# Kernel tuning notes

Measured on AMD Instinct MI355X. Metric: run time of the kernel, lower is better.

## Reference

```python
import jax, jax.numpy as jnp
import numpy as np

N = 100000
E = 1600000
D = 128


def setup_inputs() -> dict:
    key = jax.random.key(0)
    ks = jax.random.split(key, 9)
    s = 1.0 / np.sqrt(D)
    return {
        "x": jax.random.normal(ks[0], (N, D), dtype=jnp.float32),
        "edge_index": jax.random.randint(ks[1], (2, E), 0, N, dtype=jnp.int64),
        # SAGEConv layer 1: lin_l (neighbor path, with bias), lin_r (root path, no bias)
        "Wl1": jax.random.normal(ks[2], (D, D), dtype=jnp.float32) * s,
        "bl1": jnp.zeros((D,), dtype=jnp.float32),
        "Wr1": jax.random.normal(ks[3], (D, D), dtype=jnp.float32) * s,
        # SAGEConv layer 2
        "Wl2": jax.random.normal(ks[4], (D, D), dtype=jnp.float32) * s,
        "bl2": jnp.zeros((D,), dtype=jnp.float32),
        "Wr2": jax.random.normal(ks[5], (D, D), dtype=jnp.float32) * s,
    }


def _sage_conv(x, src, dst, Wl, bl, Wr):
    # PyG SAGEConv, aggr='mean', root_weight=True:
    #   out = lin_l(mean_{j in N(i)} x_j) + lin_r(x_i)
    msg = x[src]                                              # [E, D] gather
    agg = jax.ops.segment_sum(msg, dst, num_segments=N)       # [N, D]
    cnt = jax.ops.segment_sum(jnp.ones((src.shape[0],), x.dtype), dst, num_segments=N)
    agg = agg / jnp.maximum(cnt, 1.0)[:, None]                # mean aggregation
    return agg @ Wl.T + bl + x @ Wr.T


def reference(x, edge_index, Wl1, bl1, Wr1, Wl2, bl2, Wr2):
    src, dst = edge_index[0], edge_index[1]
    h = jax.nn.relu(_sage_conv(x, src, dst, Wl1, bl1, Wr1))
    out = _sage_conv(h, src, dst, Wl2, bl2, Wr2)
    return out
```

## Files before the change

### kernel.cpp

```cpp
#include <hip/hip_runtime.h>
#include <stdint.h>

#define DN 128
#define NBITS 6
#define BNODES 64
#define HBMAX 2048
#define CAP 1536
#define NSL 256

__host__ __device__ static inline int divup(int a, int b){ return (a+b-1)/b; }

typedef __attribute__((ext_vector_type(8))) short bf16x8;
typedef __attribute__((ext_vector_type(4))) float floatx4;

__device__ __forceinline__ unsigned short f2bf(float f){
  unsigned int x = __float_as_uint(f);
  unsigned int r = x + 0x7fffu + ((x >> 16) & 1u);
  return (unsigned short)(r >> 16);
}
__device__ __forceinline__ unsigned int pack2(unsigned short a, unsigned short b){
  return (unsigned int)a | ((unsigned int)b << 16);
}

__global__ __launch_bounds__(256)
void convert_scatter(const float* __restrict__ x,
                     const float* __restrict__ w0, const float* __restrict__ w1,
                     const float* __restrict__ w2, const float* __restrict__ w3,
                     unsigned short* __restrict__ xb, unsigned short* __restrict__ Wb,
                     const int* __restrict__ src, const int* __restrict__ dst,
                     int* __restrict__ gcur, unsigned int* __restrict__ packed,
                     int E, int nbuck, int count8){
  __shared__ int h[HBMAX];
  __shared__ int cur[HBMAX];
  int t = threadIdx.x;

  if (blockIdx.x < NSL){
    int s = blockIdx.x;
    for (int i=t; i<nbuck; i+=256) h[i] = 0;
    __syncthreads();
    int n4 = E >> 2, per4 = divup(n4, NSL);
    int lo = s*per4, hi = min(lo+per4, n4);
    const int4* dst4 = (const int4*)dst;
    for (int i = lo + t; i < hi; i += 256){
      int4 d4 = dst4[i];
      atomicAdd(&h[d4.x >> NBITS], 1);
      atomicAdd(&h[d4.y >> NBITS], 1);
      atomicAdd(&h[d4.z >> NBITS], 1);
      atomicAdd(&h[d4.w >> NBITS], 1);
    }
    if (s == NSL-1){
      for (int e = (n4<<2) + t; e < E; e += 256)
        atomicAdd(&h[dst[e] >> NBITS], 1);
    }
    __syncthreads();
    for (int i=t; i<nbuck; i+=256){
      int c = h[i];
      int base = c ? atomicAdd(&gcur[i], c) : 0;
      cur[i] = i*CAP + base;
    }
    __syncthreads();
    const int4* src4 = (const int4*)src;
    for (int i = lo + t; i < hi; i += 256){
      int4 d4 = dst4[i];
      int4 s4 = src4[i];
      int dd[4] = {d4.x, d4.y, d4.z, d4.w};
      int ss[4] = {s4.x, s4.y, s4.z, s4.w};
      #pragma unroll
      for (int j=0;j<4;j++){
        int d = dd[j], b = d >> NBITS;
        int pos = atomicAdd(&cur[b], 1);
        if (pos < (b+1)*CAP)
          packed[pos] = (unsigned)ss[j] | ((unsigned)(d & (BNODES-1)) << 17);
      }
    }
    if (s == NSL-1){
      for (int e = (n4<<2) + t; e < E; e += 256){
        int d = dst[e], b = d >> NBITS;
        int pos = atomicAdd(&cur[b], 1);
        if (pos < (b+1)*CAP)
          packed[pos] = (unsigned)src[e] | ((unsigned)(d & (BNODES-1)) << 17);
      }
    }
  } else {
    int i = (blockIdx.x - NSL)*256 + t;
    const float* sp; unsigned short* dp; int off;
    if (i < count8){ sp = x; dp = xb; off = i; }
    else {
      int tid = i - count8;
      if (tid >= 8192) return;
      int mat = tid >> 11; off = tid & 2047;
      sp = (mat==0)?w0:(mat==1)?w1:(mat==2)?w2:w3;
      dp = Wb + (size_t)mat*16384;
    }
    const float4* sv = (const float4*)sp + (size_t)off*2;
    float4 a = sv[0], b = sv[1];
    uint4 o;
    o.x = pack2(f2bf(a.x), f2bf(a.y));
    o.y = pack2(f2bf(a.z), f2bf(a.w));
    o.z = pack2(f2bf(b.x), f2bf(b.y));
    o.w = pack2(f2bf(b.z), f2bf(b.w));
    ((uint4*)dp)[off] = o;
  }
}

__global__ __launch_bounds__(256)
void node_sort(const int* __restrict__ gcur, unsigned int* __restrict__ buf,
               int2* __restrict__ nodeOff2, int n){
  __shared__ int cnts[BNODES], offs[BNODES], cursor[BNODES];
  int b = blockIdx.x, t = threadIdx.x;
  int cnt = min(gcur[b], CAP);
  int base = b*CAP;
  if (t < BNODES) cnts[t] = 0;
  __syncthreads();
  unsigned pk[6];
  #pragma unroll
  for (int k=0;k<6;k++){
    int i = t + k*256;
    if (i < cnt){
      pk[k] = buf[base + i];
      atomicAdd(&cnts[(pk[k]>>17)&63], 1);
    }
  }
  __syncthreads();
  if (t < BNODES){
    int v = cnts[t], sft = v;
    #pragma unroll
    for (int off=1; off<64; off<<=1){
      int u = __shfl_up(sft, off, 64);
      if (t >= off) sft += u;
    }
    offs[t] = sft - v; cursor[t] = sft - v;
    int node = b*BNODES + t;
    if (node < n) nodeOff2[node] = make_int2(base + sft - v, base + sft);
  }
  __syncthreads();
  #pragma unroll
  for (int k=0;k<6;k++){
    int i = t + k*256;
    if (i < cnt){
      int nd = (pk[k]>>17)&63;
      int r = atomicAdd(&cursor[nd], 1);
      buf[base + r] = pk[k] & 0x1FFFFu;
    }
  }
}

__global__ __launch_bounds__(256)
void aggregate_csr(const unsigned short* __restrict__ xb, const int2* __restrict__ nodeOff2,
                   const unsigned int* __restrict__ csr_src, unsigned short* __restrict__ aggb, int n){
  int g = (blockIdx.x*256 + threadIdx.x) >> 4;
  int l = threadIdx.x & 15;
  if (g >= n) return;
  int2 be = nodeOff2[g];
  int beg = be.x, end = be.y;
  float acc[8] = {0,0,0,0,0,0,0,0};
  #define ACCUM(u) { unsigned int w;                                   \
      w=(u).x; acc[0]+=__uint_as_float(w<<16); acc[1]+=__uint_as_float(w&0xffff0000u); \
      w=(u).y; acc[2]+=__uint_as_float(w<<16); acc[3]+=__uint_as_float(w&0xffff0000u); \
      w=(u).z; acc[4]+=__uint_as_float(w<<16); acc[5]+=__uint_as_float(w&0xffff0000u); \
      w=(u).w; acc[6]+=__uint_as_float(w<<16); acc[7]+=__uint_as_float(w&0xffff0000u); }
  int p = beg;
  for (; p+4 <= end; p += 4){
    int s0 = csr_src[p], s1 = csr_src[p+1], s2 = csr_src[p+2], s3 = csr_src[p+3];
    uint4 u0 = ((const uint4*)(xb + (size_t)s0*DN))[l];
    uint4 u1 = ((const uint4*)(xb + (size_t)s1*DN))[l];
    uint4 u2 = ((const uint4*)(xb + (size_t)s2*DN))[l];
    uint4 u3 = ((const uint4*)(xb + (size_t)s3*DN))[l];
    ACCUM(u0) ACCUM(u1) ACCUM(u2) ACCUM(u3)
  }
  for (; p < end; ++p){
    int s0 = csr_src[p];
    uint4 u0 = ((const uint4*)(xb + (size_t)s0*DN))[l];
    ACCUM(u0)
  }
  #undef ACCUM
  float inv = 1.f / fmaxf((float)(end-beg), 1.f);
  uint4 o;
  o.x = pack2(f2bf(acc[0]*inv), f2bf(acc[1]*inv));
  o.y = pack2(f2bf(acc[2]*inv), f2bf(acc[3]*inv));
  o.z = pack2(f2bf(acc[4]*inv), f2bf(acc[5]*inv));
  o.w = pack2(f2bf(acc[6]*inv), f2bf(acc[7]*inv));
  ((uint4*)(aggb + (size_t)g*DN))[l] = o;
}

template<bool RELU, bool OUT_BF16>
__global__ __launch_bounds__(256)
void gemm_mfma(const unsigned short* __restrict__ A1, const unsigned short* __restrict__ W1b,
               const unsigned short* __restrict__ A2, const unsigned short* __restrict__ W2b,
               const float* __restrict__ bias, void* __restrict__ out,
               int rt_total, int rt_per_block)
{
  int wave = threadIdx.x >> 6;
  int lane = threadIdx.x & 63;
  int m = lane & 15, quad = lane >> 4;

  bf16x8 Bf[2][2][4];
  {
    const unsigned short* Ws[2] = {W1b, W2b};
    #pragma unroll
    for (int c2=0;c2<2;c2++){
      int col = wave*32 + c2*16 + m;
      #pragma unroll
      for (int mat=0;mat<2;mat++){
        const unsigned short* wrow = Ws[mat] + (size_t)col*DN + quad*8;
        #pragma unroll
        for (int kc=0;kc<4;kc++)
          Bf[c2][mat][kc] = *(const bf16x8*)(wrow + kc*32);
      }
    }
  }
  float bv0 = bias[wave*32 + m];
  float bv1 = bias[wave*32 + 16 + m];

  int rt_begin = blockIdx.x * rt_per_block;
  int rt_end = rt_begin + rt_per_block; if (rt_end > rt_total) rt_end = rt_total;

  for (int rt = rt_begin; rt < rt_end; ++rt){
    const unsigned short* a1p = A1 + ((size_t)(rt*16 + m))*DN + quad*8;
    const unsigned short* a2p = A2 + ((size_t)(rt*16 + m))*DN + quad*8;
    bf16x8 Af[2][4];
    #pragma unroll
    for (int kc=0;kc<4;kc++){
      Af[0][kc] = *(const bf16x8*)(a1p + kc*32);
      Af[1][kc] = *(const bf16x8*)(a2p + kc*32);
    }
    __syncthreads();
    floatx4 acc0 = {0.f,0.f,0.f,0.f}, acc1 = {0.f,0.f,0.f,0.f};
    #pragma unroll
    for (int mat=0; mat<2; mat++)
      #pragma unroll
      for (int kc=0; kc<4; kc++){
        acc0 = __builtin_amdgcn_mfma_f32_16x16x32_bf16(Af[mat][kc], Bf[0][mat][kc], acc0, 0,0,0);
        acc1 = __builtin_amdgcn_mfma_f32_16x16x32_bf16(Af[mat][kc], Bf[1][mat][kc], acc1, 0,0,0);
      }
    #pragma unroll
    for (int r=0;r<4;r++){
      int row = rt*16 + quad*4 + r;
      float v0 = acc0[r] + bv0;
      float v1 = acc1[r] + bv1;
      if (RELU){ v0 = fmaxf(v0, 0.f); v1 = fmaxf(v1, 0.f); }
      if (OUT_BF16){
        unsigned short* o = (unsigned short*)out + (size_t)row*DN + wave*32 + m;
        o[0]  = f2bf(v0);
        o[16] = f2bf(v1);
      } else {
        float* o = (float*)out + (size_t)row*DN + wave*32 + m;
        o[0]  = v0;
        o[16] = v1;
      }
    }
  }
}


extern "C" void kernel_launch(void* const* d_in, const int* in_sizes, int n_in,
                              void* d_out, int out_size, void* d_ws, size_t ws_size,
                              hipStream_t stream) {
  const float* x   = (const float*)d_in[0];
  const int*   ei  = (const int*)d_in[1];
  const float* Wl1 = (const float*)d_in[2];
  const float* bl1 = (const float*)d_in[3];
  const float* Wr1 = (const float*)d_in[4];
  const float* Wl2 = (const float*)d_in[5];
  const float* bl2 = (const float*)d_in[6];
  const float* Wr2 = (const float*)d_in[7];

  const int n = in_sizes[0] / DN;
  const int E = in_sizes[1] / 2;
  const int* src = ei;
  const int* dst = ei + E;
  const int nbuck = divup(n, BNODES);

  char* ws = (char*)d_ws;
  char* ws_end = ws + ws_size;
  int* gcur = (int*)ws;  ws += (size_t)HBMAX*4;
  ws = (char*)(((uintptr_t)ws + 255) & ~(uintptr_t)255);
  unsigned int* packed = (unsigned int*)ws; ws += (size_t)nbuck*CAP*4;
  ws = (char*)(((uintptr_t)ws + 255) & ~(uintptr_t)255);
  int2* nodeOff2   = (int2*)ws; ws += (size_t)n*8;
  ws = (char*)(((uintptr_t)ws + 255) & ~(uintptr_t)255);
  unsigned short* Wb   = (unsigned short*)ws; ws += 4*16384*2;
  unsigned short* xb   = (unsigned short*)ws; ws += (size_t)n*DN*2;
  unsigned short* aggb = (unsigned short*)ws; ws += (size_t)n*DN*2;
  unsigned short* hb = xb;
  if (ws + (size_t)n*DN*2 <= ws_end) { hb = (unsigned short*)ws; ws += (size_t)n*DN*2; }

  unsigned short* Wl1b = Wb;
  unsigned short* Wr1b = Wb + 16384;
  unsigned short* Wl2b = Wb + 2*16384;
  unsigned short* Wr2b = Wb + 3*16384;

  const int count8 = n*DN/8;
  hipMemsetAsync(gcur, 0, (size_t)HBMAX*4, stream);
  const int cgrid = NSL + divup(count8 + 8192, 256);
  convert_scatter<<<cgrid,256,0,stream>>>(x, Wl1, Wr1, Wl2, Wr2, xb, Wb,
                                          src, dst, gcur, packed, E, nbuck, count8);
  node_sort<<<nbuck,256,0,stream>>>(gcur, packed, nodeOff2, n);

  const int rt_total = n / 16;
  const int rt_per_block = 5;
  const int gblocks = divup(rt_total, rt_per_block);
  const int agrid = divup(n*16, 256);

  aggregate_csr<<<agrid,256,0,stream>>>(xb, nodeOff2, packed, aggb, n);
  gemm_mfma<true, true ><<<gblocks,256,0,stream>>>(aggb, Wl1b, xb, Wr1b, bl1, hb, rt_total, rt_per_block);
  aggregate_csr<<<agrid,256,0,stream>>>(hb, nodeOff2, packed, aggb, n);
  gemm_mfma<false,false><<<gblocks,256,0,stream>>>(aggb, Wl2b, hb, Wr2b, bl2, d_out, rt_total, rt_per_block);
}
```

Baseline: 328.6 us.

## Apply linear transforms before mean aggregation and fuse node sort with first GEMM

Uses the linearity of mean aggregation to reorder each SAGE layer. The GEMM now runs first, producing y = x·Wlᵀ and z = x·Wrᵀ + b. The aggregation kernel then gathers and averages y, adds z, and applies ReLU/output conversion, which removes the intermediate agg buffer and the dual-input GEMM. Node-sort blocks and the first GEMM blocks share one launch since they are independent, saving a kernel launch and letting the two overlap. Final fp32 output is written with coalesced vector stores from the aggregation kernel, but bf16 rounding now happens on y before averaging, which slightly changes numerics.

```diff
diff --git a/kernel.cpp b/kernel.cpp
--- a/kernel.cpp
+++ b/kernel.cpp
@@ -103,10 +103,11 @@
   }
 }
 
-__global__ __launch_bounds__(256)
-void node_sort(const int* __restrict__ gcur, unsigned int* __restrict__ buf,
-               int2* __restrict__ nodeOff2, int n){
-  __shared__ int cnts[BNODES], offs[BNODES], cursor[BNODES];
+
+__device__ __forceinline__
+void node_sort_body(const int* __restrict__ gcur, unsigned int* __restrict__ buf,
+                    int2* __restrict__ nodeOff2, int n){
+  __shared__ int cnts[BNODES], cursor[BNODES];
   int b = blockIdx.x, t = threadIdx.x;
   int cnt = min(gcur[b], CAP);
   int base = b*CAP;
@@ -129,7 +130,7 @@
       int u = __shfl_up(sft, off, 64);
       if (t >= off) sft += u;
     }
-    offs[t] = sft - v; cursor[t] = sft - v;
+    cursor[t] = sft - v;
     int node = b*BNODES + t;
     if (node < n) nodeOff2[node] = make_int2(base + sft - v, base + sft);
   }
@@ -145,9 +146,96 @@
   }
 }
 
+__device__ __forceinline__
+void gemm_pre_body(int blk, const unsigned short* __restrict__ A,
+                   const unsigned short* __restrict__ Wlb, const unsigned short* __restrict__ Wrb,
+                   const float* __restrict__ bias,
+                   unsigned short* __restrict__ y, unsigned short* __restrict__ z,
+                   int rt_total, int rt_per_block)
+{
+  int t = threadIdx.x;
+  int wave = t >> 6, lane = t & 63;
+  int m = lane & 15, quad = lane >> 4;
+
+  bf16x8 Bf[2][2][4];
+  {
+    const unsigned short* Ws[2] = {Wlb, Wrb};
+    #pragma unroll
+    for (int c2=0;c2<2;c2++){
+      int col = wave*32 + c2*16 + m;
+      #pragma unroll
+      for (int mat=0;mat<2;mat++){
+        const unsigned short* wrow = Ws[mat] + (size_t)col*DN + quad*8;
+        #pragma unroll
+        for (int kc=0;kc<4;kc++)
+          Bf[c2][mat][kc] = *(const bf16x8*)(wrow + kc*32);
+      }
+    }
+  }
+  float bv0 = bias[wave*32 + m];
+  float bv1 = bias[wave*32 + 16 + m];
+
+  int rt_begin = blk * rt_per_block;
+  int rt_end = rt_begin + rt_per_block; if (rt_end > rt_total) rt_end = rt_total;
+
+  for (int rt = rt_begin; rt < rt_end; ++rt){
+    const unsigned short* ap = A + ((size_t)(rt*16 + m))*DN + quad*8;
+    bf16x8 Af[4];
+    #pragma unroll
+    for (int kc=0;kc<4;kc++) Af[kc] = *(const bf16x8*)(ap + kc*32);
+    __syncthreads();
+    floatx4 aY0 = {0.f,0.f,0.f,0.f}, aY1 = {0.f,0.f,0.f,0.f};
+    floatx4 aZ0 = {0.f,0.f,0.f,0.f}, aZ1 = {0.f,0.f,0.f,0.f};
+    #pragma unroll
+    for (int kc=0; kc<4; kc++){
+      aY0 = __builtin_amdgcn_mfma_f32_16x16x32_bf16(Af[kc], Bf[0][0][kc], aY0, 0,0,0);
+      aY1 = __builtin_amdgcn_mfma_f32_16x16x32_bf16(Af[kc], Bf[1][0][kc], aY1, 0,0,0);
+      aZ0 = __builtin_amdgcn_mfma_f32_16x16x32_bf16(Af[kc], Bf[0][1][kc], aZ0, 0,0,0);
+      aZ1 = __builtin_amdgcn_mfma_f32_16x16x32_bf16(Af[kc], Bf[1][1][kc], aZ1, 0,0,0);
+    }
+    #pragma unroll
+    for (int r=0;r<4;r++){
+      int row = rt*16 + quad*4 + r;
+      unsigned short* yo = y + (size_t)row*DN + wave*32 + m;
+      yo[0]  = f2bf(aY0[r]);
+      yo[16] = f2bf(aY1[r]);
+      unsigned short* zo = z + (size_t)row*DN + wave*32 + m;
+      zo[0]  = f2bf(aZ0[r] + bv0);
+      zo[16] = f2bf(aZ1[r] + bv1);
+    }
+  }
+}
+
 __global__ __launch_bounds__(256)
-void aggregate_csr(const unsigned short* __restrict__ xb, const int2* __restrict__ nodeOff2,
-                   const unsigned int* __restrict__ csr_src, unsigned short* __restrict__ aggb, int n){
+void sort_gemm1(const int* __restrict__ gcur, unsigned int* __restrict__ buf,
+                int2* __restrict__ nodeOff2, int n, int nbuck,
+                const unsigned short* __restrict__ A,
+                const unsigned short* __restrict__ Wlb, const unsigned short* __restrict__ Wrb,
+                const float* __restrict__ bias,
+                unsigned short* __restrict__ y, unsigned short* __restrict__ z,
+                int rt_total, int rt_per_block)
+{
+  if ((int)blockIdx.x < nbuck)
+    node_sort_body(gcur, buf, nodeOff2, n);
+  else
+    gemm_pre_body(blockIdx.x - nbuck, A, Wlb, Wrb, bias, y, z, rt_total, rt_per_block);
+}
+
+__global__ __launch_bounds__(256)
+void gemm_pre(const unsigned short* __restrict__ A,
+              const unsigned short* __restrict__ Wlb, const unsigned short* __restrict__ Wrb,
+              const float* __restrict__ bias,
+              unsigned short* __restrict__ y, unsigned short* __restrict__ z,
+              int rt_total, int rt_per_block)
+{
+  gemm_pre_body(blockIdx.x, A, Wlb, Wrb, bias, y, z, rt_total, rt_per_block);
+}
+
+template<bool RELU, bool OUT_BF16>
+__global__ __launch_bounds__(256)
+void aggregate_pre(const unsigned short* __restrict__ yb, const unsigned short* __restrict__ zb,
+                   const int2* __restrict__ nodeOff2, const unsigned int* __restrict__ csr_src,
+                   void* __restrict__ out, int n){
   int g = (blockIdx.x*256 + threadIdx.x) >> 4;
   int l = threadIdx.x & 15;
   if (g >= n) return;
@@ -162,93 +250,44 @@
   int p = beg;
   for (; p+4 <= end; p += 4){
     int s0 = csr_src[p], s1 = csr_src[p+1], s2 = csr_src[p+2], s3 = csr_src[p+3];
-    uint4 u0 = ((const uint4*)(xb + (size_t)s0*DN))[l];
-    uint4 u1 = ((const uint4*)(xb + (size_t)s1*DN))[l];
-    uint4 u2 = ((const uint4*)(xb + (size_t)s2*DN))[l];
-    uint4 u3 = ((const uint4*)(xb + (size_t)s3*DN))[l];
+    uint4 u0 = ((const uint4*)(yb + (size_t)s0*DN))[l];
+    uint4 u1 = ((const uint4*)(yb + (size_t)s1*DN))[l];
+    uint4 u2 = ((const uint4*)(yb + (size_t)s2*DN))[l];
+    uint4 u3 = ((const uint4*)(yb + (size_t)s3*DN))[l];
     ACCUM(u0) ACCUM(u1) ACCUM(u2) ACCUM(u3)
   }
   for (; p < end; ++p){
     int s0 = csr_src[p];
-    uint4 u0 = ((const uint4*)(xb + (size_t)s0*DN))[l];
+    uint4 u0 = ((const uint4*)(yb + (size_t)s0*DN))[l];
     ACCUM(u0)
   }
   #undef ACCUM
   float inv = 1.f / fmaxf((float)(end-beg), 1.f);
-  uint4 o;
-  o.x = pack2(f2bf(acc[0]*inv), f2bf(acc[1]*inv));
-  o.y = pack2(f2bf(acc[2]*inv), f2bf(acc[3]*inv));
-  o.z = pack2(f2bf(acc[4]*inv), f2bf(acc[5]*inv));
-  o.w = pack2(f2bf(acc[6]*inv), f2bf(acc[7]*inv));
-  ((uint4*)(aggb + (size_t)g*DN))[l] = o;
-}
-
-template<bool RELU, bool OUT_BF16>
-__global__ __launch_bounds__(256)
-void gemm_mfma(const unsigned short* __restrict__ A1, const unsigned short* __restrict__ W1b,
-               const unsigned short* __restrict__ A2, const unsigned short* __restrict__ W2b,
-               const float* __restrict__ bias, void* __restrict__ out,
-               int rt_total, int rt_per_block)
-{
-  int wave = threadIdx.x >> 6;
-  int lane = threadIdx.x & 63;
-  int m = lane & 15, quad = lane >> 4;
-
-  bf16x8 Bf[2][2][4];
-  {
-    const unsigned short* Ws[2] = {W1b, W2b};
-    #pragma unroll
-    for (int c2=0;c2<2;c2++){
-      int col = wave*32 + c2*16 + m;
-      #pragma unroll
-      for (int mat=0;mat<2;mat++){
-        const unsigned short* wrow = Ws[mat] + (size_t)col*DN + quad*8;
-        #pragma unroll
-        for (int kc=0;kc<4;kc++)
-          Bf[c2][mat][kc] = *(const bf16x8*)(wrow + kc*32);
-      }
-    }
-  }
-  float bv0 = bias[wave*32 + m];
-  float bv1 = bias[wave*32 + 16 + m];
-
-  int rt_begin = blockIdx.x * rt_per_block;
-  int rt_end = rt_begin + rt_per_block; if (rt_end > rt_total) rt_end = rt_total;
-
-  for (int rt = rt_begin; rt < rt_end; ++rt){
-    const unsigned short* a1p = A1 + ((size_t)(rt*16 + m))*DN + quad*8;
-    const unsigned short* a2p = A2 + ((size_t)(rt*16 + m))*DN + quad*8;
-    bf16x8 Af[2][4];
-    #pragma unroll
-    for (int kc=0;kc<4;kc++){
-      Af[0][kc] = *(const bf16x8*)(a1p + kc*32);
-      Af[1][kc] = *(const bf16x8*)(a2p + kc*32);
-    }
-    __syncthreads();
-    floatx4 acc0 = {0.f,0.f,0.f,0.f}, acc1 = {0.f,0.f,0.f,0.f};
-    #pragma unroll
-    for (int mat=0; mat<2; mat++)
-      #pragma unroll
-      for (int kc=0; kc<4; kc++){
-        acc0 = __builtin_amdgcn_mfma_f32_16x16x32_bf16(Af[mat][kc], Bf[0][mat][kc], acc0, 0,0,0);
-        acc1 = __builtin_amdgcn_mfma_f32_16x16x32_bf16(Af[mat][kc], Bf[1][mat][kc], acc1, 0,0,0);
-      }
-    #pragma unroll
-    for (int r=0;r<4;r++){
-      int row = rt*16 + quad*4 + r;
-      float v0 = acc0[r] + bv0;
-      float v1 = acc1[r] + bv1;
-      if (RELU){ v0 = fmaxf(v0, 0.f); v1 = fmaxf(v1, 0.f); }
-      if (OUT_BF16){
-        unsigned short* o = (unsigned short*)out + (size_t)row*DN + wave*32 + m;
-        o[0]  = f2bf(v0);
-        o[16] = f2bf(v1);
-      } else {
-        float* o = (float*)out + (size_t)row*DN + wave*32 + m;
-        o[0]  = v0;
-        o[16] = v1;
-      }
-    }
+  uint4 zc = ((const uint4*)(zb + (size_t)g*DN))[l];
+  float v[8];
+  { unsigned int w;
+    w=zc.x; v[0]=__uint_as_float(w<<16); v[1]=__uint_as_float(w&0xffff0000u);
+    w=zc.y; v[2]=__uint_as_float(w<<16); v[3]=__uint_as_float(w&0xffff0000u);
+    w=zc.z; v[4]=__uint_as_float(w<<16); v[5]=__uint_as_float(w&0xffff0000u);
+    w=zc.w; v[6]=__uint_as_float(w<<16); v[7]=__uint_as_float(w&0xffff0000u); }
+  #pragma unroll
+  for (int k=0;k<8;k++){
+    v[k] += acc[k]*inv;
+    if (RELU) v[k] = fmaxf(v[k], 0.f);
+  }
+  if (OUT_BF16){
+    uint4 o;
+    o.x = pack2(f2bf(v[0]), f2bf(v[1]));
+    o.y = pack2(f2bf(v[2]), f2bf(v[3]));
+    o.z = pack2(f2bf(v[4]), f2bf(v[5]));
+    o.w = pack2(f2bf(v[6]), f2bf(v[7]));
+    ((uint4*)((unsigned short*)out + (size_t)g*DN))[l] = o;
+  } else {
+    float* orow = (float*)out + (size_t)g*DN + l*8;
+    float4 s0 = {v[0], v[1], v[2], v[3]};
+    float4 s1 = {v[4], v[5], v[6], v[7]};
+    ((float4*)orow)[0] = s0;
+    ((float4*)orow)[1] = s1;
   }
 }
 
@@ -272,18 +311,16 @@
   const int nbuck = divup(n, BNODES);
 
   char* ws = (char*)d_ws;
-  char* ws_end = ws + ws_size;
   int* gcur = (int*)ws;  ws += (size_t)HBMAX*4;
   ws = (char*)(((uintptr_t)ws + 255) & ~(uintptr_t)255);
   unsigned int* packed = (unsigned int*)ws; ws += (size_t)nbuck*CAP*4;
   ws = (char*)(((uintptr_t)ws + 255) & ~(uintptr_t)255);
   int2* nodeOff2   = (int2*)ws; ws += (size_t)n*8;
   ws = (char*)(((uintptr_t)ws + 255) & ~(uintptr_t)255);
-  unsigned short* Wb   = (unsigned short*)ws; ws += 4*16384*2;
-  unsigned short* xb   = (unsigned short*)ws; ws += (size_t)n*DN*2;
-  unsigned short* aggb = (unsigned short*)ws; ws += (size_t)n*DN*2;
-  unsigned short* hb = xb;
-  if (ws + (size_t)n*DN*2 <= ws_end) { hb = (unsigned short*)ws; ws += (size_t)n*DN*2; }
+  unsigned short* Wb = (unsigned short*)ws; ws += 4*16384*2;
+  unsigned short* xb = (unsigned short*)ws; ws += (size_t)n*DN*2;
+  unsigned short* yb = (unsigned short*)ws; ws += (size_t)n*DN*2;
+  unsigned short* hb = (unsigned short*)ws; ws += (size_t)n*DN*2;
 
   unsigned short* Wl1b = Wb;
   unsigned short* Wr1b = Wb + 16384;
@@ -291,19 +328,19 @@
   unsigned short* Wr2b = Wb + 3*16384;
 
   const int count8 = n*DN/8;
+  const int rt_total = n / 16;
+  const int rt_per_block = 5;
+  const int gblocks = divup(rt_total, rt_per_block);
+  const int agrid = divup(n*16, 256);
+
   hipMemsetAsync(gcur, 0, (size_t)HBMAX*4, stream);
   const int cgrid = NSL + divup(count8 + 8192, 256);
   convert_scatter<<<cgrid,256,0,stream>>>(x, Wl1, Wr1, Wl2, Wr2, xb, Wb,
                                           src, dst, gcur, packed, E, nbuck, count8);
-  node_sort<<<nbuck,256,0,stream>>>(gcur, packed, nodeOff2, n);
-
-  const int rt_total = n / 16;
-  const int rt_per_block = 5;
-  const int gblocks = divup(rt_total, rt_per_block);
-  const int agrid = divup(n*16, 256);
-
-  aggregate_csr<<<agrid,256,0,stream>>>(xb, nodeOff2, packed, aggb, n);
-  gemm_mfma<true, true ><<<gblocks,256,0,stream>>>(aggb, Wl1b, xb, Wr1b, bl1, hb, rt_total, rt_per_block);
-  aggregate_csr<<<agrid,256,0,stream>>>(hb, nodeOff2, packed, aggb, n);
-  gemm_mfma<false,false><<<gblocks,256,0,stream>>>(aggb, Wl2b, hb, Wr2b, bl2, d_out, rt_total, rt_per_block);
-}
+  sort_gemm1<<<nbuck + gblocks,256,0,stream>>>(gcur, packed, nodeOff2, n, nbuck,
+                                               xb, Wl1b, Wr1b, bl1, yb, xb,
+                                               rt_total, rt_per_block);
+  aggregate_pre<true, true ><<<agrid,256,0,stream>>>(yb, xb, nodeOff2, packed, hb, n);
+  gemm_pre<<<gblocks,256,0,stream>>>(hb, Wl2b, Wr2b, bl2, yb, xb, rt_total, rt_per_block);
+  aggregate_pre<false,false><<<agrid,256,0,stream>>>(yb, xb, nodeOff2, packed, d_out, n);
+}
```

Measured after the change: 324.7 us. About the same (-1.2%).
